# Optimization experiments

Hardware: AMD Instinct MI355X
Metric: run time of the kernel (lower is better)

The kernel has to match this reference:

```python
import jax, jax.numpy as jnp
import numpy as np

T, B = 32, 64
H, W = 16, 16
FEAT = 32
CNN_DIM = 512
N_ACT = 5
MAP_OUT = FEAT * H * W  # 8192, flattened map readout


def _conv_relu(x, w, b, stride):
    y = jax.lax.conv_general_dilated(
        x, w, (stride, stride), 'VALID',
        dimension_numbers=('NCHW', 'OIHW', 'NCHW'))
    return jax.nn.relu(y + b[None, :, None, None])


def _mlp(x, w1, b1, w2, b2):
    return jax.nn.relu(x @ w1 + b1) @ w2 + b2


def setup_inputs() -> dict:
    key = jax.random.key(0)
    ks = jax.random.split(key, 32)
    g = lambda k, shape, fan: jax.random.normal(k, shape, jnp.float32) * (1.0 / np.sqrt(fan))
    inp = {}
    inp['image'] = jax.random.uniform(ks[0], (T * B, 84, 84, 3), jnp.float32) * 255.0
    inp['done'] = jnp.zeros((T, B), jnp.float32)
    inp['state0'] = jnp.zeros((B, FEAT, H, W), jnp.float32)
    inp['position'] = jax.random.randint(ks[1], (T * B, 2), 0, H).astype(jnp.int32)
    # NatureCNN params
    inp['w1'] = g(ks[2], (32, 3, 8, 8), 3 * 8 * 8); inp['b1'] = jnp.zeros((32,), jnp.float32)
    inp['w2'] = g(ks[3], (64, 32, 4, 4), 32 * 4 * 4); inp['b2'] = jnp.zeros((64,), jnp.float32)
    inp['w3'] = g(ks[4], (64, 64, 3, 3), 64 * 3 * 3); inp['b3'] = jnp.zeros((64,), jnp.float32)
    inp['wfc'] = g(ks[5], (64 * 7 * 7, CNN_DIM), 64 * 7 * 7); inp['bfc'] = jnp.zeros((CNN_DIM,), jnp.float32)
    # Map write projection
    inp['Ww'] = g(ks[6], (CNN_DIM, FEAT), CNN_DIM); inp['bw'] = jnp.zeros((FEAT,), jnp.float32)
    # pos_net MLP: one-hot(16)+one-hot(16)=32 -> 64
    inp['wp1'] = g(ks[7], (2 * H, 64), 2 * H); inp['bp1'] = jnp.zeros((64,), jnp.float32)
    inp['wp2'] = g(ks[8], (64, 64), 64); inp['bp2'] = jnp.zeros((64,), jnp.float32)
    # policy MLP: (MAP_OUT+64) -> 64 -> N_ACT
    inp['wpo1'] = g(ks[9], (MAP_OUT + 64, 64), MAP_OUT + 64); inp['bpo1'] = jnp.zeros((64,), jnp.float32)
    inp['wpo2'] = g(ks[10], (64, N_ACT), 64) * 0.01; inp['bpo2'] = jnp.zeros((N_ACT,), jnp.float32)
    # value MLP
    inp['wv1'] = g(ks[11], (MAP_OUT + 64, 64), MAP_OUT + 64); inp['bv1'] = jnp.zeros((64,), jnp.float32)
    inp['wv2'] = g(ks[12], (64, 1), 64); inp['bv2'] = jnp.zeros((1,), jnp.float32)
    return inp


def reference(image, done, state0, w1, b1, w2, b2, w3, b3, wfc, bfc, Ww, bw,
              wp1, bp1, wp2, bp2, wpo1, bpo1, wpo2, bpo2, wv1, bv1, wv2, bv2,
              position):
    # preprocess_image: /255 and NHWC -> NCHW
    x = jnp.transpose(image / 255.0, (0, 3, 1, 2))
    x = _conv_relu(x, w1, b1, 4)   # [TB,32,20,20]
    x = _conv_relu(x, w2, b2, 2)   # [TB,64,9,9]
    x = _conv_relu(x, w3, b3, 1)   # [TB,64,7,7]
    h = jax.nn.relu(x.reshape(x.shape[0], -1) @ wfc + bfc)  # [TB,512]

    h_seq = h.reshape(T, B, CNN_DIM)
    idx_seq = position.reshape(T, B, 2)
    benv = jnp.arange(B)

    def step(state, inp):
        h_t, d_t, i_t = inp
        masked = (1.0 - d_t)[:, None, None, None] * state  # reset done envs
        wfeat = h_t @ Ww + bw                              # [B,FEAT]
        state = masked.at[benv, :, i_t[:, 0], i_t[:, 1]].add(wfeat)
        return state, state.reshape(B, -1)                 # per-step map readout

    state, outs = jax.lax.scan(step, state0, (h_seq, done, idx_seq))
    hidden = outs.reshape(T * B, MAP_OUT)

    # position net on one-hot coords
    pos_oh = jnp.concatenate([jax.nn.one_hot(position[:, 0], H, dtype=hidden.dtype),
                              jax.nn.one_hot(position[:, 1], W, dtype=hidden.dtype)], axis=1)
    pos_feat = _mlp(pos_oh, wp1, bp1, wp2, bp2)            # [TB,64]
    hidden = jnp.concatenate([hidden, pos_feat], axis=1)

    logits = _mlp(hidden, wpo1, bpo1, wpo2, bpo2)          # [TB,N_ACT]
    v = _mlp(hidden, wv1, bv1, wv2, bv2)                   # [TB,1]
    return logits, v, state
```

## Files before the change

kernel.cpp:

```cpp
#include <hip/hip_runtime.h>
#include <hip/hip_bf16.h>


#define TT 32
#define BB 64
#define TBR 2048

typedef _Float16 half_t;
typedef __attribute__((ext_vector_type(4))) _Float16 half4;
typedef __attribute__((ext_vector_type(8))) _Float16 half8;
typedef __attribute__((ext_vector_type(4))) float f32x4;

#define OFF_W1T   0u
#define OFF_W2T   6144u
#define OFF_W3T   22528u
#define OFF_WF    40960u
#define OFF_PF    106496u
#define OFF_Y0    237568u
#define OFF_YS    245760u
#define OFF_H     507904u
#define OFF_DELTA 1556480u
#define OFF_WFCT  1818624u
#define OFF_C3    2621440u
#define OFF_C2    5832704u
#define OFF_C1    11141120u

__global__ __launch_bounds__(256) void prep_all(
    const float* __restrict__ w1, const float* __restrict__ w2,
    const float* __restrict__ w3, half_t* __restrict__ w1p,
    half_t* __restrict__ w2T, half_t* __restrict__ w3T,
    const float* __restrict__ wfc, half_t* __restrict__ wfcT) {
  __shared__ float t[32][33];
  int bx = blockIdx.x;
  if (bx < 304) {
    int g = bx * 256 + threadIdx.x;
    if (g < 8192) {
      int kk = g & 31, oc = (g >> 5) & 31, tap = g >> 10;
      half_t v = (half_t)0.f;
      if (kk < 24) {
        int kx = kk / 3, c = kk - 3 * kx;
        v = (half_t)(w1[oc * 192 + c * 64 + tap * 8 + kx] * (1.0f / 255.0f));
      }
      w1p[g] = v;
      return;
    }
    int g2 = g - 8192;
    if (g2 < 32768) {
      int c = g2 & 31, oc = (g2 >> 5) & 63, tap = g2 >> 11;
      w2T[g2] = (half_t)w2[oc * 512 + c * 16 + tap];
      return;
    }
    int g3 = g2 - 32768;
    if (g3 < 36864) {
      int c = g3 & 63, oc = (g3 >> 6) & 63, tap = g3 >> 12;
      w3T[g3] = (half_t)w3[oc * 576 + c * 9 + tap];
    }
    return;
  }
  int gb = bx - 304;
  int k0 = (gb % 98) * 32, n0 = (gb / 98) * 32;
  int tx = threadIdx.x & 31, ty = threadIdx.x >> 5;
#pragma unroll
  for (int i = 0; i < 4; ++i)
    t[ty + 8 * i][tx] = wfc[(size_t)(k0 + ty + 8 * i) * 512 + n0 + tx];
  __syncthreads();
#pragma unroll
  for (int i = 0; i < 4; ++i)
    wfcT[(size_t)(n0 + ty + 8 * i) * 3136 + k0 + tx] =
        (half_t)t[tx][ty + 8 * i];
}

#define C1_BANDF 5040
#define C1_BANDV 1260
__global__ __launch_bounds__(256) void conv1_mfma(
    const float* __restrict__ img, const half_t* __restrict__ w1p,
    const float* __restrict__ b1, half_t* __restrict__ out, int n0) {
  __shared__ __align__(16) half_t As[2][C1_BANDF];
  int tid = threadIdx.x;
  int li = blockIdx.x;
  int w = tid >> 6, l = tid & 63, lc = l & 15, q = l >> 4;
  const float* ib = img + (size_t)(n0 + li) * 21168;
  half_t* ob = out + (size_t)li * 400 * 32;

  half8 bfrag[8][2];
#pragma unroll
  for (int tap = 0; tap < 8; ++tap)
#pragma unroll
    for (int t = 0; t < 2; ++t)
      bfrag[tap][t] =
          *(const half8*)(w1p + (size_t)(tap * 32 + t * 16 + lc) * 32 + q * 8);
  float b1v[2] = {b1[lc], b1[16 + lc]};

  f32x4 fr[5];
#define C1_LOADB(b)                                                   \
  {                                                                   \
    const float* src = ib + 4032 * (b);                               \
    _Pragma("unroll") for (int i = 0; i < 5; ++i) {                   \
      int g = tid + 256 * i;                                          \
      if (g < C1_BANDV) fr[i] = *(const f32x4*)(src + 4 * g);         \
    }                                                                 \
  }
#define C1_WRITEB(buf)                                                \
  {                                                                   \
    _Pragma("unroll") for (int i = 0; i < 5; ++i) {                   \
      int g = tid + 256 * i;                                          \
      if (g < C1_BANDV) {                                             \
        half4 o;                                                      \
        _Pragma("unroll") for (int j = 0; j < 4; ++j)                 \
            o[j] = (half_t)fr[i][j];                                  \
        *(half4*)&As[buf][4 * g] = o;                                 \
      }                                                               \
    }                                                                 \
  }

  C1_LOADB(0);
  C1_WRITEB(0);
  for (int b = 0; b < 5; ++b) {
    if (b < 4) C1_LOADB(b + 1);
    __syncthreads();
    int buf = b & 1;
    for (int tile = w; tile < 5; tile += 4) {
      int lp = tile * 16 + lc;
      int oyl = lp / 20, ox = lp - oyl * 20;
      f32x4 acc[2];
      acc[0] = (f32x4){0.f, 0.f, 0.f, 0.f};
      acc[1] = (f32x4){0.f, 0.f, 0.f, 0.f};
#pragma unroll
      for (int ky = 0; ky < 8; ++ky) {
        half8 af;
        if (q < 3) {
          const half_t* p = &As[buf][(4 * oyl + ky) * 252 + 12 * ox + q * 8];
          *(half4*)&af = *(const half4*)p;
          *((half4*)&af + 1) = *((const half4*)(p + 4));
        } else {
#pragma unroll
          for (int j = 0; j < 8; ++j) af[j] = (half_t)0.f;
        }
        acc[0] = __builtin_amdgcn_mfma_f32_16x16x32_f16(af, bfrag[ky][0],
                                                        acc[0], 0, 0, 0);
        acc[1] = __builtin_amdgcn_mfma_f32_16x16x32_f16(af, bfrag[ky][1],
                                                        acc[1], 0, 0, 0);
      }
#pragma unroll
      for (int t = 0; t < 2; ++t) {
#pragma unroll
        for (int r = 0; r < 4; ++r) {
          int mr = b * 80 + tile * 16 + q * 4 + r;
          ob[(size_t)mr * 32 + t * 16 + lc] =
              (half_t)fmaxf(acc[t][r] + b1v[t], 0.f);
        }
      }
    }
    if (b < 4) C1_WRITEB((b + 1) & 1);
  }
}

__global__ __launch_bounds__(256) void conv2_mfma(
    const half_t* __restrict__ in, const half_t* __restrict__ w2T,
    const float* __restrict__ b2, half_t* __restrict__ out, int n0) {
  __shared__ __align__(16) half_t As[12800];
  int tid = threadIdx.x;
  int li = blockIdx.x;
  int w = tid >> 6, l = tid & 63, lc = l & 15, q = l >> 4;
  const half_t* inb = in + (size_t)li * 12800;

#pragma unroll
  for (int i = 0; i < 7; ++i) {
    int ci = tid + 256 * i;
    if (ci < 1600) {
      uint4 v = *(const uint4*)(inb + ci * 8);
      int ip = ci >> 2, sp = ip >> 1;
      int u = ((ip & 1) << 6) | ((ci & 3) << 4);
      int byte = sp * 128 + (u ^ ((sp & 7) << 4));
      *(uint4*)((char*)As + byte) = v;
    }
  }

  half8 bfrag[16][2];
#pragma unroll
  for (int tap = 0; tap < 16; ++tap)
#pragma unroll
    for (int j = 0; j < 2; ++j) {
      int nt = (w & 1) * 2 + j;
      bfrag[tap][j] =
          *(const half8*)(w2T + (size_t)(tap * 64 + nt * 16 + lc) * 32 + q * 8);
    }
  float b2v[2];
#pragma unroll
  for (int j = 0; j < 2; ++j) b2v[j] = b2[(w & 1) * 32 + j * 16 + lc];

  __syncthreads();

  half_t* ob = out + (size_t)(n0 + li) * 5184;
#pragma unroll
  for (int ti = 0; ti < 3; ++ti) {
    int tile = (w >> 1) + 2 * ti;
    int row16 = tile * 16 + lc;
    int orow = row16 < 81 ? row16 : 80;
    int oy = orow / 9, ox = orow - oy * 9;
    f32x4 acc[2];
    acc[0] = (f32x4){0.f, 0.f, 0.f, 0.f};
    acc[1] = (f32x4){0.f, 0.f, 0.f, 0.f};
#pragma unroll
    for (int tap = 0; tap < 16; ++tap) {
      int ky = tap >> 2, kx = tap & 3;
      int ip = (2 * oy + ky) * 20 + 2 * ox + kx;
      int sp = ip >> 1;
      int u = ((ip & 1) << 6) | (q << 4);
      int byte = sp * 128 + (u ^ ((sp & 7) << 4));
      half8 af = *(const half8*)((const char*)As + byte);
      acc[0] = __builtin_amdgcn_mfma_f32_16x16x32_f16(af, bfrag[tap][0],
                                                      acc[0], 0, 0, 0);
      acc[1] = __builtin_amdgcn_mfma_f32_16x16x32_f16(af, bfrag[tap][1],
                                                      acc[1], 0, 0, 0);
    }
#pragma unroll
    for (int j = 0; j < 2; ++j) {
#pragma unroll
      for (int r = 0; r < 4; ++r) {
        int mr = tile * 16 + q * 4 + r;
        if (mr < 81) {
          int col = (w & 1) * 32 + j * 16 + lc;
          ob[(size_t)mr * 64 + col] = (half_t)fmaxf(acc[j][r] + b2v[j], 0.f);
        }
      }
    }
  }
}

__global__ __launch_bounds__(256) void conv3_mfma(
    const half_t* __restrict__ in, const half_t* __restrict__ w3T,
    const float* __restrict__ b3, half_t* __restrict__ out) {
  __shared__ __align__(16) half_t As[5184];
  int tid = threadIdx.x;
  int li = blockIdx.x;
  int w = tid >> 6, l = tid & 63, lc = l & 15, q = l >> 4;
  const half_t* inb = in + (size_t)li * 5184;

#pragma unroll
  for (int i = 0; i < 3; ++i) {
    int ci = tid + 256 * i;
    if (ci < 648) {
      uint4 v = *(const uint4*)(inb + ci * 8);
      int ir = ci >> 3, cc = ci & 7;
      int byte = ir * 128 + (((cc << 4)) ^ ((ir & 7) << 4));
      *(uint4*)((char*)As + byte) = v;
    }
  }

  half8 bfrag[9][2];
#pragma unroll
  for (int tap = 0; tap < 9; ++tap)
#pragma unroll
    for (int ch = 0; ch < 2; ++ch)
      bfrag[tap][ch] = *(const half8*)(
          w3T + (size_t)(tap * 64 + w * 16 + lc) * 64 + ch * 32 + q * 8);
  float b3v = b3[w * 16 + lc];

  __syncthreads();

  half_t* ob = out + (size_t)li * 3136;
#pragma unroll
  for (int tile = 0; tile < 4; ++tile) {
    int row16 = tile * 16 + lc;
    int orow = row16 < 49 ? row16 : 48;
    int oy = orow / 7, ox = orow - oy * 7;
    f32x4 acc = (f32x4){0.f, 0.f, 0.f, 0.f};
#pragma unroll
    for (int tap = 0; tap < 9; ++tap) {
      int ky = tap / 3, kx = tap - ky * 3;
      int ir = (oy + ky) * 9 + ox + kx;
#pragma unroll
      for (int ch = 0; ch < 2; ++ch) {
        int byte = ir * 128 + (((ch << 6) | (q << 4)) ^ ((ir & 7) << 4));
        half8 af = *(const half8*)((const char*)As + byte);
        acc = __builtin_amdgcn_mfma_f32_16x16x32_f16(af, bfrag[tap][ch],
                                                     acc, 0, 0, 0);
      }
    }
#pragma unroll
    for (int r = 0; r < 4; ++r) {
      int pos = tile * 16 + q * 4 + r;
      if (pos < 49) {
        int col = w * 16 + lc;
        ob[(size_t)col * 49 + pos] = (half_t)fmaxf(acc[r] + b3v, 0.f);
      }
    }
  }
}

__global__ __launch_bounds__(256) void fc_mfma(
    const half_t* __restrict__ A, const half_t* __restrict__ Bt,
    float* __restrict__ h0, float* __restrict__ h1) {
  __shared__ __align__(16) half_t As[2][64 * 40];
  __shared__ __align__(16) half_t Bs[2][64 * 40];
  int tid = threadIdx.x;
  int m0 = blockIdx.y * 64, n0 = blockIdx.x * 64;
  int kh = blockIdx.z;
  int w = tid >> 6;
  int l = tid & 63;
  int lc = l & 15, q = l >> 4;
  int srow = tid >> 2, sseg = tid & 3;

  const half_t* aPtr = A + (size_t)(m0 + srow) * 3136 + kh * 1568 + sseg * 8;
  const half_t* bPtr = Bt + (size_t)(n0 + srow) * 3136 + kh * 1568 + sseg * 8;
  uint4 aReg = *(const uint4*)aPtr;
  uint4 bReg = *(const uint4*)bPtr;

  f32x4 acc[4];
#pragma unroll
  for (int t = 0; t < 4; ++t) acc[t] = (f32x4){0.f, 0.f, 0.f, 0.f};

  for (int s = 0; s < 49; ++s) {
    int cur = s & 1;
    *(uint4*)&As[cur][srow * 40 + sseg * 8] = aReg;
    *(uint4*)&Bs[cur][srow * 40 + sseg * 8] = bReg;
    __syncthreads();
    if (s < 48) {
      aReg = *(const uint4*)(aPtr + (s + 1) * 32);
      bReg = *(const uint4*)(bPtr + (s + 1) * 32);
    }
    half8 af = *(const half8*)&As[cur][(w * 16 + lc) * 40 + q * 8];
#pragma unroll
    for (int t = 0; t < 4; ++t) {
      half8 bf = *(const half8*)&Bs[cur][(t * 16 + lc) * 40 + q * 8];
      acc[t] = __builtin_amdgcn_mfma_f32_16x16x32_f16(af, bf, acc[t], 0, 0, 0);
    }
  }
  float* H = kh ? h1 : h0;
#pragma unroll
  for (int t = 0; t < 4; ++t) {
#pragma unroll
    for (int r = 0; r < 4; ++r) {
      int row = m0 + w * 16 + q * 4 + r;
      int col = n0 + t * 16 + lc;
      H[(size_t)row * 512 + col] = acc[t][r];
    }
  }
}

__global__ __launch_bounds__(256) void mid1_kernel(
    const float* __restrict__ h0, const float* __restrict__ h1,
    const float* __restrict__ bfc, const float* __restrict__ Ww,
    const float* __restrict__ bw, float* __restrict__ wf,
    const int* __restrict__ pos, const float* __restrict__ wp1,
    const float* __restrict__ bp1, const float* __restrict__ wp2,
    const float* __restrict__ bp2, float* __restrict__ pf,
    const float* __restrict__ s0, const float* __restrict__ wpo1,
    const float* __restrict__ wv1, float* __restrict__ y0) {
  __shared__ float red[128];
  int bx = blockIdx.x;
  if (bx < 256) {
    int g = bx * 256 + threadIdx.x;
    int row = g >> 5, oc = g & 31;
    float acc = bw[oc];
    const float* hr0 = h0 + (size_t)row * 512;
    const float* hr1 = h1 + (size_t)row * 512;
#pragma unroll 8
    for (int k = 0; k < 512; ++k)
      acc += fmaxf(hr0[k] + hr1[k] + bfc[k], 0.f) * Ww[k * 32 + oc];
    wf[g] = acc;
    return;
  }
  if (bx < 768) {
    int row = ((bx - 256) * 256 + threadIdx.x) >> 6;
    int l = threadIdx.x & 63;
    int p0 = pos[row * 2], p1 = pos[row * 2 + 1];
    float t1 = fmaxf(wp1[p0 * 64 + l] + wp1[(16 + p1) * 64 + l] + bp1[l], 0.f);
    float acc = bp2[l];
#pragma unroll
    for (int k = 0; k < 64; ++k) acc += __shfl(t1, k) * wp2[k * 64 + l];
    pf[row * 64 + l] = acc;
    return;
  }
  int g = bx - 768;
  int b = g >> 5, kc = g & 31;
  int n = threadIdx.x & 127, kh = threadIdx.x >> 7;
  const float* W = (n < 64) ? (wpo1 + n) : (wv1 + (n - 64));
  int k0 = kc * 256 + kh * 128;
  const float* s = s0 + (size_t)b * 8192 + k0;
  float acc = 0.f;
#pragma unroll 8
  for (int j = 0; j < 128; ++j) acc += s[j] * W[(size_t)(k0 + j) * 64];
  if (kh) red[n] = acc;
  __syncthreads();
  if (!kh) atomicAdd(y0 + b * 128 + n, acc + red[n]);
}

__global__ __launch_bounds__(256) void mid2_kernel(
    const int* __restrict__ pos, const float* __restrict__ wf,
    const float* __restrict__ wpo1, const float* __restrict__ wv1,
    float* __restrict__ delta, const float* __restrict__ s0,
    const float* __restrict__ done, float* __restrict__ out_state) {
  int bx = blockIdx.x;
  if (bx < 1024) {
    int row = bx * 2 + (threadIdx.x >> 7);
    int n = threadIdx.x & 127;
    const float* W = (n < 64) ? (wpo1 + n) : (wv1 + (n - 64));
    int off = pos[row * 2] * 16 + pos[row * 2 + 1];
    const float* wfr = wf + row * 32;
    float d = 0.f;
#pragma unroll
    for (int c = 0; c < 32; ++c) d += wfr[c] * W[(size_t)(c * 256 + off) * 64];
    delta[(size_t)row * 128 + n] = d;
    return;
  }
  int b = bx - 1024, tid = threadIdx.x;
  float s[32];
#pragma unroll
  for (int c = 0; c < 32; ++c) s[c] = s0[(size_t)b * 8192 + c * 256 + tid];
  for (int t = 0; t < TT; ++t) {
    int row = t * BB + b;
    float mask = 1.f - done[row];
    int off = pos[row * 2] * 16 + pos[row * 2 + 1];
#pragma unroll
    for (int c = 0; c < 32; ++c) s[c] *= mask;
    if (tid == off) {
#pragma unroll
      for (int c = 0; c < 32; ++c) s[c] += wf[row * 32 + c];
    }
  }
#pragma unroll
  for (int c = 0; c < 32; ++c) out_state[(size_t)b * 8192 + c * 256 + tid] = s[c];
}

__global__ __launch_bounds__(128) void scan_kernel(
    const float* __restrict__ y0, const float* __restrict__ done,
    const float* __restrict__ delta, float* __restrict__ ys) {
  int b = blockIdx.x;
  int n = threadIdx.x;
  float y = y0[b * 128 + n];
  for (int t = 0; t < TT; ++t) {
    int row = t * BB + b;
    y = y * (1.f - done[row]) + delta[(size_t)row * 128 + n];
    ys[(size_t)row * 128 + n] = y;
  }
}

__global__ __launch_bounds__(256) void head_kernel(
    const float* __restrict__ ys, const float* __restrict__ pf,
    const float* __restrict__ wpo1, const float* __restrict__ wv1,
    const float* __restrict__ bpo1, const float* __restrict__ bv1,
    const float* __restrict__ wpo2, const float* __restrict__ bpo2,
    const float* __restrict__ wv2, const float* __restrict__ bv2,
    float* __restrict__ logits, float* __restrict__ vout) {
  int row = (blockIdx.x * 256 + threadIdx.x) >> 6;
  int l = threadIdx.x & 63;
  float pfv = pf[row * 64 + l];
  float accp = bpo1[l] + ys[(size_t)row * 128 + l];
  float accv = bv1[l] + ys[(size_t)row * 128 + 64 + l];
#pragma unroll
  for (int k = 0; k < 64; ++k) {
    float pk = __shfl(pfv, k);
    accp += pk * wpo1[(size_t)(8192 + k) * 64 + l];
    accv += pk * wv1[(size_t)(8192 + k) * 64 + l];
  }
  float rp = fmaxf(accp, 0.f), rv = fmaxf(accv, 0.f);
#pragma unroll
  for (int a = 0; a < 5; ++a) {
    float pa = rp * wpo2[l * 5 + a];
#pragma unroll
    for (int m = 32; m >= 1; m >>= 1) pa += __shfl_xor(pa, m);
    if (l == 0) logits[row * 5 + a] = pa + bpo2[a];
  }
  float pv = rv * wv2[l];
#pragma unroll
  for (int m = 32; m >= 1; m >>= 1) pv += __shfl_xor(pv, m);
  if (l == 0) vout[row] = pv + bv2[0];
}

extern "C" void kernel_launch(void* const* d_in, const int* in_sizes, int n_in,
                              void* d_out, int out_size, void* d_ws, size_t ws_size,
                              hipStream_t stream) {
  const float* image = (const float*)d_in[0];
  const float* done = (const float*)d_in[1];
  const float* state0 = (const float*)d_in[2];
  const int* position = (const int*)d_in[3];
  const float* w1 = (const float*)d_in[4];
  const float* b1 = (const float*)d_in[5];
  const float* w2 = (const float*)d_in[6];
  const float* b2 = (const float*)d_in[7];
  const float* w3 = (const float*)d_in[8];
  const float* b3 = (const float*)d_in[9];
  const float* wfc = (const float*)d_in[10];
  const float* bfc = (const float*)d_in[11];
  const float* Ww = (const float*)d_in[12];
  const float* bw = (const float*)d_in[13];
  const float* wp1 = (const float*)d_in[14];
  const float* bp1 = (const float*)d_in[15];
  const float* wp2 = (const float*)d_in[16];
  const float* bp2 = (const float*)d_in[17];
  const float* wpo1 = (const float*)d_in[18];
  const float* bpo1 = (const float*)d_in[19];
  const float* wpo2 = (const float*)d_in[20];
  const float* bpo2 = (const float*)d_in[21];
  const float* wv1 = (const float*)d_in[22];
  const float* bv1 = (const float*)d_in[23];
  const float* wv2 = (const float*)d_in[24];
  const float* bv2 = (const float*)d_in[25];

  float* ws = (float*)d_ws;
  half_t* w1p = (half_t*)(ws + OFF_W1T);
  half_t* w2T = (half_t*)(ws + OFF_W2T);
  half_t* w3T = (half_t*)(ws + OFF_W3T);
  float* wf = ws + OFF_WF;
  float* pfb = ws + OFF_PF;
  float* y0 = ws + OFF_Y0;
  float* ysb = ws + OFF_YS;
  float* h0b = ws + OFF_H;
  float* h1b = ws + OFF_C2;
  float* deltab = ws + OFF_DELTA;
  half_t* wfcT = (half_t*)(ws + OFF_WFCT);
  half_t* c3b = (half_t*)(ws + OFF_C3);
  half_t* c2b = (half_t*)(ws + OFF_C2);
  half_t* c1b = (half_t*)(ws + OFF_C1);

  float* out = (float*)d_out;
  float* out_logits = out;
  float* out_v = out + 10240;
  float* out_state = out + 12288;

  int CS;
  if (ws_size >= (size_t)24248320 * 4) CS = 2048;
  else if (ws_size >= (size_t)17694720 * 4) CS = 1024;
  else CS = 512;
  int nc = TBR / CS;

  hipMemsetAsync(y0, 0, 8192 * sizeof(float), stream);
  prep_all<<<1872, 256, 0, stream>>>(w1, w2, w3, w1p, w2T, w3T, wfc, wfcT);

  for (int c = 0; c < nc; ++c) {
    int n0 = c * CS;
    conv1_mfma<<<CS, 256, 0, stream>>>(image, w1p, b1, c1b, n0);
    conv2_mfma<<<CS, 256, 0, stream>>>(c1b, w2T, b2, c2b, n0);
  }
  conv3_mfma<<<TBR, 256, 0, stream>>>(c2b, w3T, b3, c3b);
  fc_mfma<<<dim3(8, 32, 2), 256, 0, stream>>>(c3b, wfcT, h0b, h1b);
  mid1_kernel<<<2816, 256, 0, stream>>>(h0b, h1b, bfc, Ww, bw, wf, position,
                                        wp1, bp1, wp2, bp2, pfb, state0,
                                        wpo1, wv1, y0);
  mid2_kernel<<<1088, 256, 0, stream>>>(position, wf, wpo1, wv1, deltab,
                                        state0, done, out_state);
  scan_kernel<<<64, 128, 0, stream>>>(y0, done, deltab, ysb);
  head_kernel<<<512, 256, 0, stream>>>(ysb, pfb, wpo1, wv1, bpo1, bv1,
                                       wpo2, bpo2, wv2, bv2, out_logits, out_v);
}
```

Baseline: 450.3 us.

## Fuse conv1-3 into one LDS-resident kernel and merge scan with policy/value head

Merges the three convolution kernels into a single per-image kernel that keeps the conv1 and conv2 activations in swizzled shared memory, so the large fp16 intermediates no longer go through global memory. This also removes the chunked launch loop. Separately, the pos-feature projection moves into extra blocks of mid2, and the scan kernel now computes the head MLP inline, which eliminates the ys buffer and the separate head launch. The trade-offs are more LDS per block (about 46KB), which may reduce occupancy, and a serialized head computation inside a 64-block scan.

```diff
diff --git a/kernel.cpp b/kernel.cpp
--- a/kernel.cpp
+++ b/kernel.cpp
@@ -17,13 +17,12 @@
 #define OFF_WF    40960u
 #define OFF_PF    106496u
 #define OFF_Y0    237568u
-#define OFF_YS    245760u
+#define OFF_PP    245760u
 #define OFF_H     507904u
 #define OFF_DELTA 1556480u
 #define OFF_WFCT  1818624u
 #define OFF_C3    2621440u
-#define OFF_C2    5832704u
-#define OFF_C1    11141120u
+#define OFF_H1    5832704u
 
 __global__ __launch_bounds__(256) void prep_all(
     const float* __restrict__ w1, const float* __restrict__ w2,
@@ -72,22 +71,31 @@
 
 #define C1_BANDF 5040
 #define C1_BANDV 1260
-__global__ __launch_bounds__(256) void conv1_mfma(
+#define C1OUT_OFF 20672
+#define C1A(ip, bp)                                                     \
+  (C1OUT_OFF + ((ip) >> 1) * 128 +                                      \
+   (((((ip) & 1) << 6) | ((bp) & 0x30)) ^ ((((ip) >> 1) & 7) << 4)) +   \
+   ((bp) & 15))
+#define C2A(ir, bp) \
+  ((ir) * 128 + (((bp) & 0x70) ^ (((ir) & 7) << 4)) + ((bp) & 15))
+__global__ __launch_bounds__(256) void conv123_mfma(
     const float* __restrict__ img, const half_t* __restrict__ w1p,
-    const float* __restrict__ b1, half_t* __restrict__ out, int n0) {
-  __shared__ __align__(16) half_t As[2][C1_BANDF];
+    const float* __restrict__ b1, const half_t* __restrict__ w2T,
+    const float* __restrict__ b2, const half_t* __restrict__ w3T,
+    const float* __restrict__ b3, half_t* __restrict__ out) {
+  __shared__ __align__(16) char lds[46272];
+  half_t (*stag)[C1_BANDF] = (half_t(*)[C1_BANDF])lds;
   int tid = threadIdx.x;
   int li = blockIdx.x;
   int w = tid >> 6, l = tid & 63, lc = l & 15, q = l >> 4;
-  const float* ib = img + (size_t)(n0 + li) * 21168;
-  half_t* ob = out + (size_t)li * 400 * 32;
-
-  half8 bfrag[8][2];
+  const float* ib = img + (size_t)li * 21168;
+
+  half8 bfrag1[8][2];
 #pragma unroll
   for (int tap = 0; tap < 8; ++tap)
 #pragma unroll
     for (int t = 0; t < 2; ++t)
-      bfrag[tap][t] =
+      bfrag1[tap][t] =
           *(const half8*)(w1p + (size_t)(tap * 32 + t * 16 + lc) * 32 + q * 8);
   float b1v[2] = {b1[lc], b1[16 + lc]};
 
@@ -108,7 +116,7 @@
         half4 o;                                                      \
         _Pragma("unroll") for (int j = 0; j < 4; ++j)                 \
             o[j] = (half_t)fr[i][j];                                  \
-        *(half4*)&As[buf][4 * g] = o;                                 \
+        *(half4*)&stag[buf][4 * g] = o;                               \
       }                                                               \
     }                                                                 \
   }
@@ -129,161 +137,117 @@
       for (int ky = 0; ky < 8; ++ky) {
         half8 af;
         if (q < 3) {
-          const half_t* p = &As[buf][(4 * oyl + ky) * 252 + 12 * ox + q * 8];
+          const half_t* p = &stag[buf][(4 * oyl + ky) * 252 + 12 * ox + q * 8];
           *(half4*)&af = *(const half4*)p;
           *((half4*)&af + 1) = *((const half4*)(p + 4));
         } else {
 #pragma unroll
           for (int j = 0; j < 8; ++j) af[j] = (half_t)0.f;
         }
-        acc[0] = __builtin_amdgcn_mfma_f32_16x16x32_f16(af, bfrag[ky][0],
+        acc[0] = __builtin_amdgcn_mfma_f32_16x16x32_f16(af, bfrag1[ky][0],
                                                         acc[0], 0, 0, 0);
-        acc[1] = __builtin_amdgcn_mfma_f32_16x16x32_f16(af, bfrag[ky][1],
+        acc[1] = __builtin_amdgcn_mfma_f32_16x16x32_f16(af, bfrag1[ky][1],
                                                         acc[1], 0, 0, 0);
       }
 #pragma unroll
       for (int t = 0; t < 2; ++t) {
 #pragma unroll
         for (int r = 0; r < 4; ++r) {
-          int mr = b * 80 + tile * 16 + q * 4 + r;
-          ob[(size_t)mr * 32 + t * 16 + lc] =
+          int ip = b * 80 + tile * 16 + q * 4 + r;
+          int ch = t * 16 + lc;
+          *(half_t*)(lds + C1A(ip, 2 * ch)) =
               (half_t)fmaxf(acc[t][r] + b1v[t], 0.f);
         }
       }
     }
     if (b < 4) C1_WRITEB((b + 1) & 1);
   }
-}
-
-__global__ __launch_bounds__(256) void conv2_mfma(
-    const half_t* __restrict__ in, const half_t* __restrict__ w2T,
-    const float* __restrict__ b2, half_t* __restrict__ out, int n0) {
-  __shared__ __align__(16) half_t As[12800];
-  int tid = threadIdx.x;
-  int li = blockIdx.x;
-  int w = tid >> 6, l = tid & 63, lc = l & 15, q = l >> 4;
-  const half_t* inb = in + (size_t)li * 12800;
-
-#pragma unroll
-  for (int i = 0; i < 7; ++i) {
-    int ci = tid + 256 * i;
-    if (ci < 1600) {
-      uint4 v = *(const uint4*)(inb + ci * 8);
-      int ip = ci >> 2, sp = ip >> 1;
-      int u = ((ip & 1) << 6) | ((ci & 3) << 4);
-      int byte = sp * 128 + (u ^ ((sp & 7) << 4));
-      *(uint4*)((char*)As + byte) = v;
-    }
-  }
-
-  half8 bfrag[16][2];
-#pragma unroll
-  for (int tap = 0; tap < 16; ++tap)
-#pragma unroll
-    for (int j = 0; j < 2; ++j) {
-      int nt = (w & 1) * 2 + j;
-      bfrag[tap][j] =
-          *(const half8*)(w2T + (size_t)(tap * 64 + nt * 16 + lc) * 32 + q * 8);
-    }
-  float b2v[2];
-#pragma unroll
-  for (int j = 0; j < 2; ++j) b2v[j] = b2[(w & 1) * 32 + j * 16 + lc];
-
   __syncthreads();
 
-  half_t* ob = out + (size_t)(n0 + li) * 5184;
-#pragma unroll
-  for (int ti = 0; ti < 3; ++ti) {
-    int tile = (w >> 1) + 2 * ti;
-    int row16 = tile * 16 + lc;
-    int orow = row16 < 81 ? row16 : 80;
-    int oy = orow / 9, ox = orow - oy * 9;
-    f32x4 acc[2];
-    acc[0] = (f32x4){0.f, 0.f, 0.f, 0.f};
-    acc[1] = (f32x4){0.f, 0.f, 0.f, 0.f};
-#pragma unroll
-    for (int tap = 0; tap < 16; ++tap) {
-      int ky = tap >> 2, kx = tap & 3;
-      int ip = (2 * oy + ky) * 20 + 2 * ox + kx;
-      int sp = ip >> 1;
-      int u = ((ip & 1) << 6) | (q << 4);
-      int byte = sp * 128 + (u ^ ((sp & 7) << 4));
-      half8 af = *(const half8*)((const char*)As + byte);
-      acc[0] = __builtin_amdgcn_mfma_f32_16x16x32_f16(af, bfrag[tap][0],
-                                                      acc[0], 0, 0, 0);
-      acc[1] = __builtin_amdgcn_mfma_f32_16x16x32_f16(af, bfrag[tap][1],
-                                                      acc[1], 0, 0, 0);
-    }
-#pragma unroll
-    for (int j = 0; j < 2; ++j) {
+  {
+    half8 bfrag2[16][2];
+#pragma unroll
+    for (int tap = 0; tap < 16; ++tap)
+#pragma unroll
+      for (int j = 0; j < 2; ++j) {
+        int nt = (w & 1) * 2 + j;
+        bfrag2[tap][j] = *(const half8*)(
+            w2T + (size_t)(tap * 64 + nt * 16 + lc) * 32 + q * 8);
+      }
+    float b2v[2];
+#pragma unroll
+    for (int j = 0; j < 2; ++j) b2v[j] = b2[(w & 1) * 32 + j * 16 + lc];
+
+#pragma unroll
+    for (int ti = 0; ti < 3; ++ti) {
+      int tile = (w >> 1) + 2 * ti;
+      int row16 = tile * 16 + lc;
+      int orow = row16 < 81 ? row16 : 80;
+      int oy = orow / 9, ox = orow - oy * 9;
+      f32x4 acc[2];
+      acc[0] = (f32x4){0.f, 0.f, 0.f, 0.f};
+      acc[1] = (f32x4){0.f, 0.f, 0.f, 0.f};
+#pragma unroll
+      for (int tap = 0; tap < 16; ++tap) {
+        int ky = tap >> 2, kx = tap & 3;
+        int ip = (2 * oy + ky) * 20 + 2 * ox + kx;
+        half8 af = *(const half8*)(lds + C1A(ip, q * 16));
+        acc[0] = __builtin_amdgcn_mfma_f32_16x16x32_f16(af, bfrag2[tap][0],
+                                                        acc[0], 0, 0, 0);
+        acc[1] = __builtin_amdgcn_mfma_f32_16x16x32_f16(af, bfrag2[tap][1],
+                                                        acc[1], 0, 0, 0);
+      }
+#pragma unroll
+      for (int j = 0; j < 2; ++j) {
+#pragma unroll
+        for (int r = 0; r < 4; ++r) {
+          int mr = tile * 16 + q * 4 + r;
+          if (mr < 81) {
+            int col = (w & 1) * 32 + j * 16 + lc;
+            *(half_t*)(lds + C2A(mr, 2 * col)) =
+                (half_t)fmaxf(acc[j][r] + b2v[j], 0.f);
+          }
+        }
+      }
+    }
+  }
+  __syncthreads();
+
+  {
+    half8 bfrag3[9][2];
+#pragma unroll
+    for (int tap = 0; tap < 9; ++tap)
+#pragma unroll
+      for (int ch = 0; ch < 2; ++ch)
+        bfrag3[tap][ch] = *(const half8*)(
+            w3T + (size_t)(tap * 64 + w * 16 + lc) * 64 + ch * 32 + q * 8);
+    float b3v = b3[w * 16 + lc];
+
+    half_t* ob = out + (size_t)li * 3136;
+#pragma unroll
+    for (int tile = 0; tile < 4; ++tile) {
+      int row16 = tile * 16 + lc;
+      int orow = row16 < 49 ? row16 : 48;
+      int oy = orow / 7, ox = orow - oy * 7;
+      f32x4 acc = (f32x4){0.f, 0.f, 0.f, 0.f};
+#pragma unroll
+      for (int tap = 0; tap < 9; ++tap) {
+        int ky = tap / 3, kx = tap - ky * 3;
+        int ir = (oy + ky) * 9 + ox + kx;
+#pragma unroll
+        for (int ch = 0; ch < 2; ++ch) {
+          half8 af = *(const half8*)(lds + C2A(ir, ch * 64 + q * 16));
+          acc = __builtin_amdgcn_mfma_f32_16x16x32_f16(af, bfrag3[tap][ch],
+                                                       acc, 0, 0, 0);
+        }
+      }
 #pragma unroll
       for (int r = 0; r < 4; ++r) {
-        int mr = tile * 16 + q * 4 + r;
-        if (mr < 81) {
-          int col = (w & 1) * 32 + j * 16 + lc;
-          ob[(size_t)mr * 64 + col] = (half_t)fmaxf(acc[j][r] + b2v[j], 0.f);
+        int pos = tile * 16 + q * 4 + r;
+        if (pos < 49) {
+          int col = w * 16 + lc;
+          ob[(size_t)col * 49 + pos] = (half_t)fmaxf(acc[r] + b3v, 0.f);
         }
-      }
-    }
-  }
-}
-
-__global__ __launch_bounds__(256) void conv3_mfma(
-    const half_t* __restrict__ in, const half_t* __restrict__ w3T,
-    const float* __restrict__ b3, half_t* __restrict__ out) {
-  __shared__ __align__(16) half_t As[5184];
-  int tid = threadIdx.x;
-  int li = blockIdx.x;
-  int w = tid >> 6, l = tid & 63, lc = l & 15, q = l >> 4;
-  const half_t* inb = in + (size_t)li * 5184;
-
-#pragma unroll
-  for (int i = 0; i < 3; ++i) {
-    int ci = tid + 256 * i;
-    if (ci < 648) {
-      uint4 v = *(const uint4*)(inb + ci * 8);
-      int ir = ci >> 3, cc = ci & 7;
-      int byte = ir * 128 + (((cc << 4)) ^ ((ir & 7) << 4));
-      *(uint4*)((char*)As + byte) = v;
-    }
-  }
-
-  half8 bfrag[9][2];
-#pragma unroll
-  for (int tap = 0; tap < 9; ++tap)
-#pragma unroll
-    for (int ch = 0; ch < 2; ++ch)
-      bfrag[tap][ch] = *(const half8*)(
-          w3T + (size_t)(tap * 64 + w * 16 + lc) * 64 + ch * 32 + q * 8);
-  float b3v = b3[w * 16 + lc];
-
-  __syncthreads();
-
-  half_t* ob = out + (size_t)li * 3136;
-#pragma unroll
-  for (int tile = 0; tile < 4; ++tile) {
-    int row16 = tile * 16 + lc;
-    int orow = row16 < 49 ? row16 : 48;
-    int oy = orow / 7, ox = orow - oy * 7;
-    f32x4 acc = (f32x4){0.f, 0.f, 0.f, 0.f};
-#pragma unroll
-    for (int tap = 0; tap < 9; ++tap) {
-      int ky = tap / 3, kx = tap - ky * 3;
-      int ir = (oy + ky) * 9 + ox + kx;
-#pragma unroll
-      for (int ch = 0; ch < 2; ++ch) {
-        int byte = ir * 128 + (((ch << 6) | (q << 4)) ^ ((ir & 7) << 4));
-        half8 af = *(const half8*)((const char*)As + byte);
-        acc = __builtin_amdgcn_mfma_f32_16x16x32_f16(af, bfrag[tap][ch],
-                                                     acc, 0, 0, 0);
-      }
-    }
-#pragma unroll
-    for (int r = 0; r < 4; ++r) {
-      int pos = tile * 16 + q * 4 + r;
-      if (pos < 49) {
-        int col = w * 16 + lc;
-        ob[(size_t)col * 49 + pos] = (half_t)fmaxf(acc[r] + b3v, 0.f);
       }
     }
   }
@@ -391,7 +355,8 @@
     const int* __restrict__ pos, const float* __restrict__ wf,
     const float* __restrict__ wpo1, const float* __restrict__ wv1,
     float* __restrict__ delta, const float* __restrict__ s0,
-    const float* __restrict__ done, float* __restrict__ out_state) {
+    const float* __restrict__ done, float* __restrict__ out_state,
+    const float* __restrict__ pf, float* __restrict__ pp) {
   int bx = blockIdx.x;
   if (bx < 1024) {
     int row = bx * 2 + (threadIdx.x >> 7);
@@ -405,68 +370,75 @@
     delta[(size_t)row * 128 + n] = d;
     return;
   }
-  int b = bx - 1024, tid = threadIdx.x;
-  float s[32];
-#pragma unroll
-  for (int c = 0; c < 32; ++c) s[c] = s0[(size_t)b * 8192 + c * 256 + tid];
-  for (int t = 0; t < TT; ++t) {
-    int row = t * BB + b;
-    float mask = 1.f - done[row];
-    int off = pos[row * 2] * 16 + pos[row * 2 + 1];
-#pragma unroll
-    for (int c = 0; c < 32; ++c) s[c] *= mask;
-    if (tid == off) {
-#pragma unroll
-      for (int c = 0; c < 32; ++c) s[c] += wf[row * 32 + c];
-    }
-  }
-#pragma unroll
-  for (int c = 0; c < 32; ++c) out_state[(size_t)b * 8192 + c * 256 + tid] = s[c];
-}
-
-__global__ __launch_bounds__(128) void scan_kernel(
+  if (bx < 1088) {
+    int b = bx - 1024, tid = threadIdx.x;
+    float s[32];
+#pragma unroll
+    for (int c = 0; c < 32; ++c) s[c] = s0[(size_t)b * 8192 + c * 256 + tid];
+    for (int t = 0; t < TT; ++t) {
+      int row = t * BB + b;
+      float mask = 1.f - done[row];
+      int off = pos[row * 2] * 16 + pos[row * 2 + 1];
+#pragma unroll
+      for (int c = 0; c < 32; ++c) s[c] *= mask;
+      if (tid == off) {
+#pragma unroll
+        for (int c = 0; c < 32; ++c) s[c] += wf[row * 32 + c];
+      }
+    }
+#pragma unroll
+    for (int c = 0; c < 32; ++c)
+      out_state[(size_t)b * 8192 + c * 256 + tid] = s[c];
+    return;
+  }
+  int row = (bx - 1088) * 2 + (threadIdx.x >> 7);
+  int n = threadIdx.x & 127;
+  const float* W = (n < 64) ? (wpo1 + n) : (wv1 + (n - 64));
+  const float* pfr = pf + row * 64;
+  float acc = 0.f;
+#pragma unroll
+  for (int k = 0; k < 64; ++k) acc += pfr[k] * W[(size_t)(8192 + k) * 64];
+  pp[(size_t)row * 128 + n] = acc;
+}
+
+__global__ __launch_bounds__(128) void scan_head_kernel(
     const float* __restrict__ y0, const float* __restrict__ done,
-    const float* __restrict__ delta, float* __restrict__ ys) {
+    const float* __restrict__ delta, const float* __restrict__ pp,
+    const float* __restrict__ bpo1, const float* __restrict__ bv1,
+    const float* __restrict__ wpo2, const float* __restrict__ bpo2,
+    const float* __restrict__ wv2, const float* __restrict__ bv2,
+    float* __restrict__ logits, float* __restrict__ vout) {
   int b = blockIdx.x;
   int n = threadIdx.x;
+  int l = n & 63, wv = n >> 6;
+  float bias1 = wv ? bv1[l] : bpo1[l];
+  float w2v[5];
+  if (!wv) {
+#pragma unroll
+    for (int a = 0; a < 5; ++a) w2v[a] = wpo2[l * 5 + a];
+  } else {
+    w2v[0] = wv2[l];
+  }
   float y = y0[b * 128 + n];
   for (int t = 0; t < TT; ++t) {
     int row = t * BB + b;
     y = y * (1.f - done[row]) + delta[(size_t)row * 128 + n];
-    ys[(size_t)row * 128 + n] = y;
-  }
-}
-
-__global__ __launch_bounds__(256) void head_kernel(
-    const float* __restrict__ ys, const float* __restrict__ pf,
-    const float* __restrict__ wpo1, const float* __restrict__ wv1,
-    const float* __restrict__ bpo1, const float* __restrict__ bv1,
-    const float* __restrict__ wpo2, const float* __restrict__ bpo2,
-    const float* __restrict__ wv2, const float* __restrict__ bv2,
-    float* __restrict__ logits, float* __restrict__ vout) {
-  int row = (blockIdx.x * 256 + threadIdx.x) >> 6;
-  int l = threadIdx.x & 63;
-  float pfv = pf[row * 64 + l];
-  float accp = bpo1[l] + ys[(size_t)row * 128 + l];
-  float accv = bv1[l] + ys[(size_t)row * 128 + 64 + l];
-#pragma unroll
-  for (int k = 0; k < 64; ++k) {
-    float pk = __shfl(pfv, k);
-    accp += pk * wpo1[(size_t)(8192 + k) * 64 + l];
-    accv += pk * wv1[(size_t)(8192 + k) * 64 + l];
-  }
-  float rp = fmaxf(accp, 0.f), rv = fmaxf(accv, 0.f);
-#pragma unroll
-  for (int a = 0; a < 5; ++a) {
-    float pa = rp * wpo2[l * 5 + a];
-#pragma unroll
-    for (int m = 32; m >= 1; m >>= 1) pa += __shfl_xor(pa, m);
-    if (l == 0) logits[row * 5 + a] = pa + bpo2[a];
-  }
-  float pv = rv * wv2[l];
-#pragma unroll
-  for (int m = 32; m >= 1; m >>= 1) pv += __shfl_xor(pv, m);
-  if (l == 0) vout[row] = pv + bv2[0];
+    float act = fmaxf(y + pp[(size_t)row * 128 + n] + bias1, 0.f);
+    if (!wv) {
+#pragma unroll
+      for (int a = 0; a < 5; ++a) {
+        float pa = act * w2v[a];
+#pragma unroll
+        for (int m = 32; m >= 1; m >>= 1) pa += __shfl_xor(pa, m);
+        if (l == 0) logits[row * 5 + a] = pa + bpo2[a];
+      }
+    } else {
+      float pv = act * w2v[0];
+#pragma unroll
+      for (int m = 32; m >= 1; m >>= 1) pv += __shfl_xor(pv, m);
+      if (l == 0) vout[row] = pv + bv2[0];
+    }
+  }
 }
 
 extern "C" void kernel_launch(void* const* d_in, const int* in_sizes, int n_in,
@@ -506,42 +478,28 @@
   float* wf = ws + OFF_WF;
   float* pfb = ws + OFF_PF;
   float* y0 = ws + OFF_Y0;
-  float* ysb = ws + OFF_YS;
+  float* ppb = ws + OFF_PP;
   float* h0b = ws + OFF_H;
-  float* h1b = ws + OFF_C2;
+  float* h1b = ws + OFF_H1;
   float* deltab = ws + OFF_DELTA;
   half_t* wfcT = (half_t*)(ws + OFF_WFCT);
   half_t* c3b = (half_t*)(ws + OFF_C3);
-  half_t* c2b = (half_t*)(ws + OFF_C2);
-  half_t* c1b = (half_t*)(ws + OFF_C1);
 
   float* out = (float*)d_out;
   float* out_logits = out;
   float* out_v = out + 10240;
   float* out_state = out + 12288;
 
-  int CS;
-  if (ws_size >= (size_t)24248320 * 4) CS = 2048;
-  else if (ws_size >= (size_t)17694720 * 4) CS = 1024;
-  else CS = 512;
-  int nc = TBR / CS;
-
   hipMemsetAsync(y0, 0, 8192 * sizeof(float), stream);
   prep_all<<<1872, 256, 0, stream>>>(w1, w2, w3, w1p, w2T, w3T, wfc, wfcT);
-
-  for (int c = 0; c < nc; ++c) {
-    int n0 = c * CS;
-    conv1_mfma<<<CS, 256, 0, stream>>>(image, w1p, b1, c1b, n0);
-    conv2_mfma<<<CS, 256, 0, stream>>>(c1b, w2T, b2, c2b, n0);
-  }
-  conv3_mfma<<<TBR, 256, 0, stream>>>(c2b, w3T, b3, c3b);
+  conv123_mfma<<<TBR, 256, 0, stream>>>(image, w1p, b1, w2T, b2, w3T, b3, c3b);
   fc_mfma<<<dim3(8, 32, 2), 256, 0, stream>>>(c3b, wfcT, h0b, h1b);
   mid1_kernel<<<2816, 256, 0, stream>>>(h0b, h1b, bfc, Ww, bw, wf, position,
                                         wp1, bp1, wp2, bp2, pfb, state0,
                                         wpo1, wv1, y0);
-  mid2_kernel<<<1088, 256, 0, stream>>>(position, wf, wpo1, wv1, deltab,
-                                        state0, done, out_state);
-  scan_kernel<<<64, 128, 0, stream>>>(y0, done, deltab, ysb);
-  head_kernel<<<512, 256, 0, stream>>>(ysb, pfb, wpo1, wv1, bpo1, bv1,
-                                       wpo2, bpo2, wv2, bv2, out_logits, out_v);
-}
+  mid2_kernel<<<2112, 256, 0, stream>>>(position, wf, wpo1, wv1, deltab,
+                                        state0, done, out_state, pfb, ppb);
+  scan_head_kernel<<<64, 128, 0, stream>>>(y0, done, deltab, ppb, bpo1, bv1,
+                                           wpo2, bpo2, wv2, bv2,
+                                           out_logits, out_v);
+}
```

New measurement: 451.7 us. No clear change (+0.3%).
